# Kernel tuning notes

Measured on AMD Instinct MI355X. Metric: run time of the kernel, lower is better.

## Reference

```python
import jax, jax.numpy as jnp
import numpy as np

POOLING_COUNTS = [15, 8, 8]
N_GRID = 64


def _build_plan(pooling_counts, n):
    """Return list of (kernel_size, conv_stride, i_idx, j_idx) matching torch module order."""
    plan = []
    stride, offset = 1, 0
    for gi, c in enumerate(pooling_counts):
        for k in range(c):
            offset += stride
            i = np.arange(0, n - offset, stride)
            j = np.arange(offset, n, stride)
            ksz = 3 if (gi > 0 and k == 0) else 2
            cstride = 2 if ksz == 3 else 1
            plan.append((ksz, cstride, i, j))
        stride *= 2
    return plan


def _conv1d(x, w, b, stride):
    # x: [B, C, L], w: [O, I, K]
    y = jax.lax.conv_general_dilated(
        x, w, window_strides=(stride,), padding='VALID',
        dimension_numbers=('NCH', 'OIH', 'NCH'))
    return y + b[None, :, None]


def setup_inputs() -> dict:
    key = jax.random.key(0)
    ks = jax.random.split(key, 5)
    H = 256
    x = jax.random.normal(ks[0], (32, H, N_GRID), dtype=jnp.float32)
    w2 = jax.random.normal(ks[1], (29, H, H, 2), dtype=jnp.float32) * 0.03
    b2 = jnp.zeros((29, H), dtype=jnp.float32)
    w3 = jax.random.normal(ks[2], (2, H, H, 3), dtype=jnp.float32) * 0.03
    b3 = jnp.zeros((2, H), dtype=jnp.float32)
    vis_w = jax.random.normal(ks[3], (H, 3 * H), dtype=jnp.float32) * 0.03
    vis_b = jnp.zeros((H,), dtype=jnp.float32)
    return {"x": x, "w2": w2, "b2": b2, "w3": w3, "b3": b3,
            "vis_w": vis_w, "vis_b": vis_b}


def reference(x, w2, b2, w3, b3, vis_w, vis_b):
    plan = _build_plan(POOLING_COUNTS, N_GRID)
    B, D, n = x.shape
    diag = np.arange(n)
    src = x
    map2d = jnp.zeros((B, 3 * D, n, n), dtype=x.dtype)
    map2d = map2d.at[:, :, diag, diag].set(jnp.tile(x, (1, 3, 1)))
    cur = x
    i2 = i3 = 0
    for ksz, cstride, ii, jj in plan:
        if ksz == 2:
            w, b = w2[i2], b2[i2]; i2 += 1
        else:
            w, b = w3[i3], b3[i3]; i3 += 1
        cur = _conv1d(cur, w, b, cstride)          # [B, D, len(ii)]
        feat = jnp.concatenate([src[:, :, ii], cur, src[:, :, jj]], axis=1)
        map2d = map2d.at[:, :, ii, jj].set(feat)
    # 1x1 Conv2d(3D -> D)
    out = jnp.einsum('bcij,oc->boij', map2d, vis_w) + vis_b[None, :, None, None]
    return out
```

## Files before the change

### kernel.cpp

```cpp
#include <hip/hip_runtime.h>

#define BB 32
#define NSTEP 31
#define CROW 1040
#define CB_STRIDE 266240L
#define XB_STRIDE 16384L
#define PPART 524288L

static const int h_lens[NSTEP] = {63,62,61,60,59,58,57,56,55,54,53,52,51,50,49,
                                  24,23,22,21,20,19,18,17,
                                  8,7,6,5,4,3,2,1};
static const int h_cb[NSTEP]   = {0,63,125,186,246,305,363,420,476,531,585,638,690,741,791,
                                  840,864,887,909,930,950,969,987,
                                  1004,1012,1019,1025,1030,1034,1037,1039};

__device__ __constant__ int d_cb[NSTEP] = {0,63,125,186,246,305,363,420,476,531,585,638,690,741,791,
                                           840,864,887,909,930,950,969,987,
                                           1004,1012,1019,1025,1030,1034,1037,1039};

typedef short v8s __attribute__((ext_vector_type(8)));
typedef float v4f __attribute__((ext_vector_type(4)));

__device__ __forceinline__ unsigned short rne_bf16(float f) {
    unsigned int u = __float_as_uint(f);
    u = (u + 0x7FFFu + ((u >> 16) & 1u)) >> 16;
    return (unsigned short)u;
}

__global__ __launch_bounds__(256)
void prep(const float* __restrict__ x, const float* __restrict__ w2,
          const float* __restrict__ w3, const float* __restrict__ vw,
          unsigned short* __restrict__ xb, unsigned short* __restrict__ w2t,
          unsigned short* __restrict__ w3t, unsigned short* __restrict__ vwb)
{
    long idx = (long)blockIdx.x * 256 + threadIdx.x;
    if (idx < 524288) {
        const int ci = idx & 255, l = (idx >> 8) & 63, b = (int)(idx >> 14);
        xb[idx] = rne_bf16(x[((long)b << 14) + ((long)ci << 6) + l]);
        return;
    }
    idx -= 524288;
    if (idx < 3801088) {
        const int ci = idx & 255, k = (idx >> 8) & 1; const long row = idx >> 9;
        w2t[idx] = rne_bf16(w2[row * 512 + ci * 2 + k]);
        return;
    }
    idx -= 3801088;
    if (idx < 393216) {
        const int ci = idx & 255; const long r = idx >> 8;
        const int k = (int)(r % 3); const long row = r / 3;
        w3t[idx] = rne_bf16(w3[row * 768 + ci * 3 + k]);
        return;
    }
    idx -= 393216;
    if (idx < 196608) vwb[idx] = rne_bf16(vw[idx]);
}

template<int KC, int S, int OMODE>
__global__ __launch_bounds__(256)
void mg(const unsigned short* __restrict__ A, int arow, int acol0,
        const unsigned short* __restrict__ B, long bbstr, int brow0,
        const float* __restrict__ bias,
        void* __restrict__ OUT, int orow0)
{
    const int lane = threadIdx.x & 63;
    const int wave = threadIdx.x >> 6;
    const int nl = lane & 15, g = lane >> 4;
    const int n = blockIdx.x * 16 + nl;
    const int b = n & 31;
    const int l = n >> 5;
    const int p = blockIdx.y;

    const unsigned short* Ab = A + (size_t)(wave * 64 + nl) * arow + acol0 + p * 256 + g * 8;
    const unsigned short* Bb = B + (size_t)b * bbstr + (size_t)(brow0 + l * S) * 256 + g * 8;

    v4f acc[4] = {};
    #pragma unroll
    for (int k = 0; k < KC * 8; ++k) {
        const v8s bf = *(const v8s*)(Bb + k * 32);
        #pragma unroll
        for (int mf = 0; mf < 4; ++mf) {
            const v8s af = *(const v8s*)(Ab + (size_t)mf * 16 * arow + k * 32);
            acc[mf] = __builtin_amdgcn_mfma_f32_16x16x32_bf16(af, bf, acc[mf], 0, 0, 0);
        }
    }

    #pragma unroll
    for (int mf = 0; mf < 4; ++mf) {
        const int m0 = wave * 64 + mf * 16 + g * 4;
        if constexpr (OMODE == 0) {
            const float4 bv = *(const float4*)(bias + m0);
            ushort4 pk;
            pk.x = rne_bf16(acc[mf][0] + bv.x);
            pk.y = rne_bf16(acc[mf][1] + bv.y);
            pk.z = rne_bf16(acc[mf][2] + bv.z);
            pk.w = rne_bf16(acc[mf][3] + bv.w);
            *(ushort4*)((unsigned short*)OUT + (size_t)b * CB_STRIDE + (size_t)(orow0 + l) * 256 + m0) = pk;
        } else if constexpr (OMODE == 1) {
            *(v4f*)((float*)OUT + (size_t)b * CB_STRIDE + (size_t)l * 256 + m0) = acc[mf];
        } else {
            float* Po = (float*)OUT + (size_t)p * PPART + (size_t)b * XB_STRIDE + l;
            #pragma unroll
            for (int r = 0; r < 4; ++r) Po[(size_t)(m0 + r) * 64] = acc[mf][r];
        }
    }
}

__global__ __launch_bounds__(256)
void final_k(const float* __restrict__ P, const float* __restrict__ Qb,
             const float* __restrict__ vb, float* __restrict__ out)
{
    const int b = blockIdx.x >> 6;
    const int i = blockIdx.x & 63;
    const int t = threadIdx.x;
    const int j = t & 63;
    const int os = t >> 6;

    __shared__ int qidx[64];
    if (t < 64) {
        const int d = t - i;
        int v = -1;
        if (t == i) v = -2;
        else if (d >= 1 && d <= 15) v = d_cb[d-1] + i;
        else if (d >= 17 && d <= 31 && (d & 1) && !(i & 1)) v = d_cb[15 + ((d-17)>>1)] + (i>>1);
        else if (d >= 35 && d <= 63 && ((d-35)&3)==0 && !(i&3)) v = d_cb[23 + ((d-35)>>2)] + (i>>2);
        qidx[t] = v;
    }
    __syncthreads();
    const int q = qidx[j];

    for (int oc = 0; oc < 64; ++oc) {
        const int o = oc * 4 + os;
        const float pl = P[(size_t)(b * 256 + o) * 64 + i];
        const float pm = P[524288u + (size_t)(b * 256 + o) * 64 + i];
        const float* pr = P + 1048576u + (size_t)(b * 256 + o) * 64;
        const float vbv = vb[o];
        float v;
        if (q == -2)      v = pl + pm + pr[i] + vbv;
        else if (q >= 0)  v = pl + Qb[(size_t)b * CB_STRIDE + (size_t)q * 256 + o] + pr[j] + vbv;
        else              v = vbv;
        out[(((size_t)b * 256 + o) * 64 + i) * 64 + j] = v;
    }
}

extern "C" void kernel_launch(void* const* d_in, const int* in_sizes, int n_in,
                              void* d_out, int out_size, void* d_ws, size_t ws_size,
                              hipStream_t stream)
{
    const float* x   = (const float*)d_in[0];
    const float* w2  = (const float*)d_in[1];
    const float* b2  = (const float*)d_in[2];
    const float* w3  = (const float*)d_in[3];
    const float* b3  = (const float*)d_in[4];
    const float* vw  = (const float*)d_in[5];
    const float* vb  = (const float*)d_in[6];
    float* out = (float*)d_out;

    char* w = (char*)d_ws;
    float*          Qf  = (float*)w;                  w += (size_t)BB * CB_STRIDE * 4;
    float*          P   = (float*)w;                  w += (size_t)3 * PPART * 4;
    unsigned short* Cb  = (unsigned short*)w;         w += (size_t)BB * CB_STRIDE * 2;
    unsigned short* xb  = (unsigned short*)w;         w += (size_t)BB * XB_STRIDE * 2;
    unsigned short* w2t = (unsigned short*)w;         w += (size_t)29 * 256 * 512 * 2;
    unsigned short* w3t = (unsigned short*)w;         w += (size_t)2 * 256 * 768 * 2;
    unsigned short* vwb = (unsigned short*)w;

    prep<<<dim3(19200), 256, 0, stream>>>(x, w2, w3, vw, xb, w2t, w3t, vwb);

    mg<1,1,2><<<dim3(128, 3), 256, 0, stream>>>(vwb, 768, 0, xb, XB_STRIDE, 0, nullptr, P, 0);

    int i2 = 0, i3 = 0;
    for (int t = 0; t < NSTEP; ++t) {
        const int L = h_lens[t];
        const unsigned short* Bsrc = (t == 0) ? xb : Cb;
        const long bst  = (t == 0) ? XB_STRIDE : CB_STRIDE;
        const int brow0 = (t == 0) ? 0 : h_cb[t-1];
        if (t == 15 || t == 23) {
            mg<3,2,0><<<dim3(2*L, 1), 256, 0, stream>>>(
                w3t + (size_t)i3 * 196608, 768, 0, Bsrc, bst, brow0,
                b3 + i3 * 256, Cb, h_cb[t]);
            ++i3;
        } else {
            mg<2,1,0><<<dim3(2*L, 1), 256, 0, stream>>>(
                w2t + (size_t)i2 * 131072, 512, 0, Bsrc, bst, brow0,
                b2 + i2 * 256, Cb, h_cb[t]);
            ++i2;
        }
    }

    mg<1,1,1><<<dim3(2080, 1), 256, 0, stream>>>(vwb, 768, 256, Cb, CB_STRIDE, 0, nullptr, Qf, 0);

    final_k<<<dim3(BB * 64), 256, 0, stream>>>(P, Qf, vb, out);
}
```

Before: 625.7 us.

## Fuse the conv chain, P and Q GEMMs into one persistent per-batch kernel

Replaces the 31 per-step conv launches plus the separate P and Q GEMM launches with a single kernel: one 1024-thread block per batch element. The block keeps its activations in double-buffered, XOR-swizzled LDS and runs every conv step and its Q projection in place. This removes launch overhead and the global round trips of intermediate activations. The cost is that only 32 blocks run, which underuses the GPU's compute units and serialises the steps within each block.

```diff
diff --git a/kernel.cpp b/kernel.cpp
--- a/kernel.cpp
+++ b/kernel.cpp
@@ -4,16 +4,11 @@
 #define NSTEP 31
 #define CROW 1040
 #define CB_STRIDE 266240L
-#define XB_STRIDE 16384L
 #define PPART 524288L
 
-static const int h_lens[NSTEP] = {63,62,61,60,59,58,57,56,55,54,53,52,51,50,49,
-                                  24,23,22,21,20,19,18,17,
-                                  8,7,6,5,4,3,2,1};
-static const int h_cb[NSTEP]   = {0,63,125,186,246,305,363,420,476,531,585,638,690,741,791,
-                                  840,864,887,909,930,950,969,987,
-                                  1004,1012,1019,1025,1030,1034,1037,1039};
-
+__device__ __constant__ int d_lens[NSTEP] = {63,62,61,60,59,58,57,56,55,54,53,52,51,50,49,
+                                             24,23,22,21,20,19,18,17,
+                                             8,7,6,5,4,3,2,1};
 __device__ __constant__ int d_cb[NSTEP] = {0,63,125,186,246,305,363,420,476,531,585,638,690,741,791,
                                            840,864,887,909,930,950,969,987,
                                            1004,1012,1019,1025,1030,1034,1037,1039};
@@ -56,53 +51,155 @@
     if (idx < 196608) vwb[idx] = rne_bf16(vw[idx]);
 }
 
-template<int KC, int S, int OMODE>
-__global__ __launch_bounds__(256)
-void mg(const unsigned short* __restrict__ A, int arow, int acol0,
-        const unsigned short* __restrict__ B, long bbstr, int brow0,
-        const float* __restrict__ bias,
-        void* __restrict__ OUT, int orow0)
-{
-    const int lane = threadIdx.x & 63;
-    const int wave = threadIdx.x >> 6;
-    const int nl = lane & 15, g = lane >> 4;
-    const int n = blockIdx.x * 16 + nl;
-    const int b = n & 31;
-    const int l = n >> 5;
-    const int p = blockIdx.y;
-
-    const unsigned short* Ab = A + (size_t)(wave * 64 + nl) * arow + acol0 + p * 256 + g * 8;
-    const unsigned short* Bb = B + (size_t)b * bbstr + (size_t)(brow0 + l * S) * 256 + g * 8;
-
-    v4f acc[4] = {};
-    #pragma unroll
-    for (int k = 0; k < KC * 8; ++k) {
-        const v8s bf = *(const v8s*)(Bb + k * 32);
+
+template<int KC, int S>
+__device__ __forceinline__ void conv_step(
+    const unsigned short* __restrict__ Wt, const float* __restrict__ bias,
+    const char* __restrict__ in, char* __restrict__ out,
+    int L, int wave, int nl, int g)
+{
+    const int nt = (L + 15) >> 4;
+    v4f acc[4] = {{0,0,0,0},{0,0,0,0},{0,0,0,0},{0,0,0,0}};
+    int lv[4];
+    #pragma unroll
+    for (int j = 0; j < 4; ++j) lv[j] = min(j * 16 + nl, L - 1);
+
+    const unsigned short* Arow = Wt + (size_t)(wave * 16 + nl) * (KC * 256) + g * 8;
+    #pragma unroll
+    for (int ki = 0; ki < KC * 8; ++ki) {
+        const int kk = ki * 32;
+        const v8s af = *(const v8s*)(Arow + kk);
         #pragma unroll
-        for (int mf = 0; mf < 4; ++mf) {
-            const v8s af = *(const v8s*)(Ab + (size_t)mf * 16 * arow + k * 32);
-            acc[mf] = __builtin_amdgcn_mfma_f32_16x16x32_bf16(af, bf, acc[mf], 0, 0, 0);
-        }
-    }
-
-    #pragma unroll
-    for (int mf = 0; mf < 4; ++mf) {
-        const int m0 = wave * 64 + mf * 16 + g * 4;
-        if constexpr (OMODE == 0) {
-            const float4 bv = *(const float4*)(bias + m0);
+        for (int j = 0; j < 4; ++j) {
+            if (j < nt) {
+                const int ir = lv[j] * S + (kk >> 8);
+                const v8s bf = *(const v8s*)(in + ir * 512 +
+                                (((kk & 255) * 2 + g * 16) ^ ((ir & 7) << 4)));
+                acc[j] = __builtin_amdgcn_mfma_f32_16x16x32_bf16(af, bf, acc[j], 0, 0, 0);
+            }
+        }
+    }
+    const int m0 = wave * 16 + g * 4;
+    const float4 bv = *(const float4*)(bias + m0);
+    #pragma unroll
+    for (int j = 0; j < 4; ++j) {
+        const int l = j * 16 + nl;
+        if (j < nt && l < L) {
             ushort4 pk;
-            pk.x = rne_bf16(acc[mf][0] + bv.x);
-            pk.y = rne_bf16(acc[mf][1] + bv.y);
-            pk.z = rne_bf16(acc[mf][2] + bv.z);
-            pk.w = rne_bf16(acc[mf][3] + bv.w);
-            *(ushort4*)((unsigned short*)OUT + (size_t)b * CB_STRIDE + (size_t)(orow0 + l) * 256 + m0) = pk;
-        } else if constexpr (OMODE == 1) {
-            *(v4f*)((float*)OUT + (size_t)b * CB_STRIDE + (size_t)l * 256 + m0) = acc[mf];
+            pk.x = rne_bf16(acc[j][0] + bv.x);
+            pk.y = rne_bf16(acc[j][1] + bv.y);
+            pk.z = rne_bf16(acc[j][2] + bv.z);
+            pk.w = rne_bf16(acc[j][3] + bv.w);
+            *(ushort4*)(out + l * 512 + ((m0 * 2) ^ ((l & 7) << 4))) = pk;
+        }
+    }
+}
+
+__device__ __forceinline__ void q_step(
+    const unsigned short* __restrict__ vwb,
+    const char* __restrict__ act, float* __restrict__ Qf,
+    int b, int row0, int L, int wave, int nl, int g)
+{
+    const int nt = (L + 15) >> 4;
+    v4f acc[4] = {{0,0,0,0},{0,0,0,0},{0,0,0,0},{0,0,0,0}};
+    int lv[4];
+    #pragma unroll
+    for (int j = 0; j < 4; ++j) lv[j] = min(j * 16 + nl, L - 1);
+
+    const unsigned short* Arow = vwb + (size_t)(wave * 16 + nl) * 768 + 256 + g * 8;
+    #pragma unroll
+    for (int ki = 0; ki < 8; ++ki) {
+        const int kk = ki * 32;
+        const v8s af = *(const v8s*)(Arow + kk);
+        #pragma unroll
+        for (int j = 0; j < 4; ++j) {
+            if (j < nt) {
+                const int ir = lv[j];
+                const v8s bf = *(const v8s*)(act + ir * 512 +
+                                ((kk * 2 + g * 16) ^ ((ir & 7) << 4)));
+                acc[j] = __builtin_amdgcn_mfma_f32_16x16x32_bf16(af, bf, acc[j], 0, 0, 0);
+            }
+        }
+    }
+    const int m0 = wave * 16 + g * 4;
+    #pragma unroll
+    for (int j = 0; j < 4; ++j) {
+        const int l = j * 16 + nl;
+        if (j < nt && l < L)
+            *(v4f*)(Qf + (size_t)b * CB_STRIDE + (size_t)(row0 + l) * 256 + m0) = acc[j];
+    }
+}
+
+__global__ __launch_bounds__(1024, 4)
+void chain(const unsigned short* __restrict__ xb,
+           const unsigned short* __restrict__ w2t,
+           const unsigned short* __restrict__ w3t,
+           const unsigned short* __restrict__ vwb,
+           const float* __restrict__ b2, const float* __restrict__ b3,
+           float* __restrict__ Qf, float* __restrict__ P)
+{
+    __shared__ unsigned short lds[2][64][256];
+    const int b = blockIdx.x;
+    const int tid = threadIdx.x;
+    const int wave = tid >> 6, lane = tid & 63, nl = lane & 15, g = lane >> 4;
+
+    char* base = (char*)&lds[0][0][0];
+
+    {
+        const unsigned short* src = xb + (size_t)b * 16384;
+        #pragma unroll
+        for (int i = 0; i < 2; ++i) {
+            const int c = tid + i * 1024;
+            const int r = c >> 5, cc = c & 31;
+            const v8s v = *(const v8s*)(src + r * 256 + cc * 8);
+            *(v8s*)(base + r * 512 + ((cc * 16) ^ ((r & 7) << 4))) = v;
+        }
+    }
+    __syncthreads();
+
+    {
+        const char* in = base;
+        for (int p = 0; p < 3; ++p) {
+            v4f acc[4] = {{0,0,0,0},{0,0,0,0},{0,0,0,0},{0,0,0,0}};
+            #pragma unroll
+            for (int ki = 0; ki < 8; ++ki) {
+                const int kk = ki * 32;
+                const v8s af = *(const v8s*)(vwb + (size_t)(wave * 16 + nl) * 768 + p * 256 + kk + g * 8);
+                #pragma unroll
+                for (int j = 0; j < 4; ++j) {
+                    const int l = j * 16 + nl;
+                    const v8s bf = *(const v8s*)(in + l * 512 +
+                                    ((kk * 2 + g * 16) ^ ((l & 7) << 4)));
+                    acc[j] = __builtin_amdgcn_mfma_f32_16x16x32_bf16(af, bf, acc[j], 0, 0, 0);
+                }
+            }
+            const int m0 = wave * 16 + g * 4;
+            #pragma unroll
+            for (int j = 0; j < 4; ++j) {
+                float* po = P + (size_t)p * PPART + (size_t)b * 16384 + j * 16 + nl;
+                #pragma unroll
+                for (int r = 0; r < 4; ++r) po[(size_t)(m0 + r) * 64] = acc[j][r];
+            }
+        }
+    }
+
+    int cur = 0, i2 = 0, i3 = 0;
+    for (int t = 0; t < NSTEP; ++t) {
+        const int L = d_lens[t];
+        char* inb  = base + cur * 32768;
+        char* outb = base + (cur ^ 1) * 32768;
+        if (t == 15 || t == 23) {
+            conv_step<3, 2>(w3t + (size_t)i3 * 196608, b3 + i3 * 256,
+                            inb, outb, L, wave, nl, g);
+            ++i3;
         } else {
-            float* Po = (float*)OUT + (size_t)p * PPART + (size_t)b * XB_STRIDE + l;
-            #pragma unroll
-            for (int r = 0; r < 4; ++r) Po[(size_t)(m0 + r) * 64] = acc[mf][r];
-        }
+            conv_step<2, 1>(w2t + (size_t)i2 * 131072, b2 + i2 * 256,
+                            inb, outb, L, wave, nl, g);
+            ++i2;
+        }
+        __syncthreads();
+        q_step(vwb, outb, Qf, b, d_cb[t], L, wave, nl, g);
+        cur ^= 1;
     }
 }
 
@@ -157,38 +254,14 @@
     float* out = (float*)d_out;
 
     char* w = (char*)d_ws;
-    float*          Qf  = (float*)w;                  w += (size_t)BB * CB_STRIDE * 4;
-    float*          P   = (float*)w;                  w += (size_t)3 * PPART * 4;
-    unsigned short* Cb  = (unsigned short*)w;         w += (size_t)BB * CB_STRIDE * 2;
-    unsigned short* xb  = (unsigned short*)w;         w += (size_t)BB * XB_STRIDE * 2;
-    unsigned short* w2t = (unsigned short*)w;         w += (size_t)29 * 256 * 512 * 2;
-    unsigned short* w3t = (unsigned short*)w;         w += (size_t)2 * 256 * 768 * 2;
+    float*          Qf  = (float*)w;          w += (size_t)BB * CB_STRIDE * 4;
+    float*          P   = (float*)w;          w += (size_t)3 * PPART * 4;
+    unsigned short* xb  = (unsigned short*)w; w += (size_t)BB * 16384 * 2;
+    unsigned short* w2t = (unsigned short*)w; w += (size_t)29 * 131072 * 2;
+    unsigned short* w3t = (unsigned short*)w; w += (size_t)2 * 196608 * 2;
     unsigned short* vwb = (unsigned short*)w;
 
     prep<<<dim3(19200), 256, 0, stream>>>(x, w2, w3, vw, xb, w2t, w3t, vwb);
-
-    mg<1,1,2><<<dim3(128, 3), 256, 0, stream>>>(vwb, 768, 0, xb, XB_STRIDE, 0, nullptr, P, 0);
-
-    int i2 = 0, i3 = 0;
-    for (int t = 0; t < NSTEP; ++t) {
-        const int L = h_lens[t];
-        const unsigned short* Bsrc = (t == 0) ? xb : Cb;
-        const long bst  = (t == 0) ? XB_STRIDE : CB_STRIDE;
-        const int brow0 = (t == 0) ? 0 : h_cb[t-1];
-        if (t == 15 || t == 23) {
-            mg<3,2,0><<<dim3(2*L, 1), 256, 0, stream>>>(
-                w3t + (size_t)i3 * 196608, 768, 0, Bsrc, bst, brow0,
-                b3 + i3 * 256, Cb, h_cb[t]);
-            ++i3;
-        } else {
-            mg<2,1,0><<<dim3(2*L, 1), 256, 0, stream>>>(
-                w2t + (size_t)i2 * 131072, 512, 0, Bsrc, bst, brow0,
-                b2 + i2 * 256, Cb, h_cb[t]);
-            ++i2;
-        }
-    }
-
-    mg<1,1,1><<<dim3(2080, 1), 256, 0, stream>>>(vwb, 768, 256, Cb, CB_STRIDE, 0, nullptr, Qf, 0);
-
+    chain<<<dim3(BB), 1024, 0, stream>>>(xb, w2t, w3t, vwb, b2, b3, Qf, P);
     final_k<<<dim3(BB * 64), 256, 0, stream>>>(P, Qf, vb, out);
 }
```

Result: slower. 812.5 us (+29.9%).

## Fuse 31-step conv chain into one persistent per-batch kernel with LDS ping-pong

Applied to the files above, without the earlier changes.

Replaces the 31 separate conv launches with a single kernel that runs one 1024-thread block per batch element, keeping the activation sequence in double-buffered LDS and iterating all steps with block barriers. Each step still writes its bf16 output to global Cb for the later 1x1 projection. This removes per-step launch overhead and global round-trips for the chain input, but uses only 32 blocks on a many-CU GPU and has every block re-read all weights from global/L2.

```diff
diff --git a/kernel.cpp b/kernel.cpp
--- a/kernel.cpp
+++ b/kernel.cpp
@@ -6,14 +6,12 @@
 #define CB_STRIDE 266240L
 #define XB_STRIDE 16384L
 #define PPART 524288L
-
-static const int h_lens[NSTEP] = {63,62,61,60,59,58,57,56,55,54,53,52,51,50,49,
-                                  24,23,22,21,20,19,18,17,
-                                  8,7,6,5,4,3,2,1};
-static const int h_cb[NSTEP]   = {0,63,125,186,246,305,363,420,476,531,585,638,690,741,791,
-                                  840,864,887,909,930,950,969,987,
-                                  1004,1012,1019,1025,1030,1034,1037,1039};
-
+#define RS 528
+#define BUF (64 * RS)
+
+__device__ __constant__ int d_lens[NSTEP] = {63,62,61,60,59,58,57,56,55,54,53,52,51,50,49,
+                                             24,23,22,21,20,19,18,17,
+                                             8,7,6,5,4,3,2,1};
 __device__ __constant__ int d_cb[NSTEP] = {0,63,125,186,246,305,363,420,476,531,585,638,690,741,791,
                                            840,864,887,909,930,950,969,987,
                                            1004,1012,1019,1025,1030,1034,1037,1039};
@@ -25,6 +23,12 @@
     unsigned int u = __float_as_uint(f);
     u = (u + 0x7FFFu + ((u >> 16) & 1u)) >> 16;
     return (unsigned short)u;
+}
+
+#define MFMA16 __builtin_amdgcn_mfma_f32_16x16x32_bf16
+
+__device__ __forceinline__ void lds_barrier() {
+    asm volatile("s_waitcnt lgkmcnt(0)\n\ts_barrier" ::: "memory");
 }
 
 __global__ __launch_bounds__(256)
@@ -56,12 +60,181 @@
     if (idx < 196608) vwb[idx] = rne_bf16(vw[idx]);
 }
 
-template<int KC, int S, int OMODE>
+
+template<int KC, int S>
+__device__ __forceinline__ void conv_big(
+    const unsigned short* __restrict__ Wt, const float* __restrict__ bias,
+    const char* in, char* out, unsigned short* __restrict__ Cbp,
+    int L, int wave, int nl, int g)
+{
+    const int wm = wave >> 1;
+    const int lg2 = wave & 1;
+    const int l0 = lg2 * 32 + nl, l1 = l0 + 16;
+    const int lv0 = min(l0, L - 1), lv1 = min(l1, L - 1);
+
+    v4f a00 = {0,0,0,0}, a01 = {0,0,0,0}, a10 = {0,0,0,0}, a11 = {0,0,0,0};
+    const unsigned short* A0 = Wt + (size_t)(wm * 32 + nl) * (KC * 256) + g * 8;
+    const unsigned short* A1 = A0 + (size_t)16 * (KC * 256);
+
+    #pragma unroll
+    for (int c = 0; c < KC; ++c) {
+        v8s wf0[8], wf1[8];
+        #pragma unroll
+        for (int k = 0; k < 8; ++k) {
+            wf0[k] = *(const v8s*)(A0 + (c * 8 + k) * 32);
+            wf1[k] = *(const v8s*)(A1 + (c * 8 + k) * 32);
+        }
+        const char* rp0 = in + (lv0 * S + c) * RS + g * 16;
+        const char* rp1 = in + (lv1 * S + c) * RS + g * 16;
+        #pragma unroll
+        for (int k = 0; k < 8; ++k) {
+            const v8s b0 = *(const v8s*)(rp0 + k * 64);
+            const v8s b1 = *(const v8s*)(rp1 + k * 64);
+            a00 = MFMA16(wf0[k], b0, a00, 0, 0, 0);
+            a10 = MFMA16(wf1[k], b0, a10, 0, 0, 0);
+            a01 = MFMA16(wf0[k], b1, a01, 0, 0, 0);
+            a11 = MFMA16(wf1[k], b1, a11, 0, 0, 0);
+        }
+    }
+    const int m0 = wm * 32 + g * 4;
+    const float4 bv0 = *(const float4*)(bias + m0);
+    const float4 bv1 = *(const float4*)(bias + m0 + 16);
+    #pragma unroll
+    for (int li = 0; li < 2; ++li) {
+        const int l = li ? l1 : l0;
+        if (l < L) {
+            const v4f aa = li ? a01 : a00;
+            const v4f ab = li ? a11 : a10;
+            ushort4 p0, p1;
+            p0.x = rne_bf16(aa[0] + bv0.x); p0.y = rne_bf16(aa[1] + bv0.y);
+            p0.z = rne_bf16(aa[2] + bv0.z); p0.w = rne_bf16(aa[3] + bv0.w);
+            p1.x = rne_bf16(ab[0] + bv1.x); p1.y = rne_bf16(ab[1] + bv1.y);
+            p1.z = rne_bf16(ab[2] + bv1.z); p1.w = rne_bf16(ab[3] + bv1.w);
+            *(ushort4*)(out + l * RS + m0 * 2) = p0;
+            *(ushort4*)(out + l * RS + (m0 + 16) * 2) = p1;
+            *(ushort4*)(Cbp + (size_t)l * 256 + m0) = p0;
+            *(ushort4*)(Cbp + (size_t)l * 256 + m0 + 16) = p1;
+        }
+    }
+}
+
+template<int KC, int S, bool TWO_L>
+__device__ __forceinline__ void conv_small(
+    const unsigned short* __restrict__ Wt, const float* __restrict__ bias,
+    const char* in, char* out, unsigned short* __restrict__ Cbp,
+    int L, int wave, int nl, int g)
+{
+    const int lv0 = min(nl, L - 1);
+    const int lv1 = min(16 + nl, L - 1);
+
+    v4f a0 = {0,0,0,0}, a1 = {0,0,0,0};
+    const unsigned short* A0 = Wt + (size_t)(wave * 16 + nl) * (KC * 256) + g * 8;
+
+    #pragma unroll
+    for (int c = 0; c < KC; ++c) {
+        v8s wf[8];
+        #pragma unroll
+        for (int k = 0; k < 8; ++k)
+            wf[k] = *(const v8s*)(A0 + (c * 8 + k) * 32);
+        const char* rp0 = in + (lv0 * S + c) * RS + g * 16;
+        const char* rp1 = in + (lv1 * S + c) * RS + g * 16;
+        #pragma unroll
+        for (int k = 0; k < 8; ++k) {
+            const v8s b0 = *(const v8s*)(rp0 + k * 64);
+            a0 = MFMA16(wf[k], b0, a0, 0, 0, 0);
+            if (TWO_L) {
+                const v8s b1 = *(const v8s*)(rp1 + k * 64);
+                a1 = MFMA16(wf[k], b1, a1, 0, 0, 0);
+            }
+        }
+    }
+    const int m0 = wave * 16 + g * 4;
+    const float4 bv = *(const float4*)(bias + m0);
+    {
+        const int l = nl;
+        if (l < L) {
+            ushort4 pk;
+            pk.x = rne_bf16(a0[0] + bv.x); pk.y = rne_bf16(a0[1] + bv.y);
+            pk.z = rne_bf16(a0[2] + bv.z); pk.w = rne_bf16(a0[3] + bv.w);
+            *(ushort4*)(out + l * RS + m0 * 2) = pk;
+            *(ushort4*)(Cbp + (size_t)l * 256 + m0) = pk;
+        }
+    }
+    if (TWO_L) {
+        const int l = 16 + nl;
+        if (l < L) {
+            ushort4 pk;
+            pk.x = rne_bf16(a1[0] + bv.x); pk.y = rne_bf16(a1[1] + bv.y);
+            pk.z = rne_bf16(a1[2] + bv.z); pk.w = rne_bf16(a1[3] + bv.w);
+            *(ushort4*)(out + l * RS + m0 * 2) = pk;
+            *(ushort4*)(Cbp + (size_t)l * 256 + m0) = pk;
+        }
+    }
+}
+
+__global__ __launch_bounds__(1024, 4)
+void chain(const unsigned short* __restrict__ xb,
+           const unsigned short* __restrict__ w2t,
+           const unsigned short* __restrict__ w3t,
+           const float* __restrict__ b2, const float* __restrict__ b3,
+           unsigned short* __restrict__ Cb)
+{
+    __shared__ __align__(16) char lds[2 * BUF];
+    const int b = blockIdx.x;
+    const int tid = threadIdx.x;
+    const int wave = tid >> 6, lane = tid & 63, nl = lane & 15, g = lane >> 4;
+
+    char* base = lds;
+
+    {
+        const unsigned short* src = xb + (size_t)b * XB_STRIDE;
+        #pragma unroll
+        for (int i = 0; i < 2; ++i) {
+            const int c = tid + i * 1024;
+            const int r = c >> 5, cc = c & 31;
+            const v8s v = *(const v8s*)(src + r * 256 + cc * 8);
+            *(v8s*)(base + r * RS + cc * 16) = v;
+        }
+    }
+    lds_barrier();
+
+    unsigned short* Cbb = Cb + (size_t)b * CB_STRIDE;
+    int cur = 0, i2 = 0, i3 = 0;
+    for (int t = 0; t < NSTEP; ++t) {
+        const int L = d_lens[t];
+        char* inb  = base + cur * BUF;
+        char* outb = base + (cur ^ 1) * BUF;
+        unsigned short* Cbp = Cbb + (size_t)d_cb[t] * 256;
+        if (t < 15) {
+            conv_big<2, 1>(w2t + (size_t)i2 * 131072, b2 + i2 * 256,
+                           inb, outb, Cbp, L, wave, nl, g);
+            ++i2;
+        } else if (t == 15) {
+            conv_small<3, 2, true>(w3t, b3, inb, outb, Cbp, L, wave, nl, g);
+            ++i3;
+        } else if (t < 23) {
+            conv_small<2, 1, true>(w2t + (size_t)i2 * 131072, b2 + i2 * 256,
+                                   inb, outb, Cbp, L, wave, nl, g);
+            ++i2;
+        } else if (t == 23) {
+            conv_small<3, 2, false>(w3t + 196608, b3 + 256,
+                                    inb, outb, Cbp, L, wave, nl, g);
+            ++i3;
+        } else {
+            conv_small<2, 1, false>(w2t + (size_t)i2 * 131072, b2 + i2 * 256,
+                                    inb, outb, Cbp, L, wave, nl, g);
+            ++i2;
+        }
+        lds_barrier();
+        cur ^= 1;
+    }
+}
+
+template<int OMODE>
 __global__ __launch_bounds__(256)
 void mg(const unsigned short* __restrict__ A, int arow, int acol0,
-        const unsigned short* __restrict__ B, long bbstr, int brow0,
-        const float* __restrict__ bias,
-        void* __restrict__ OUT, int orow0)
+        const unsigned short* __restrict__ B, long bbstr,
+        void* __restrict__ OUT)
 {
     const int lane = threadIdx.x & 63;
     const int wave = threadIdx.x >> 6;
@@ -72,31 +245,22 @@
     const int p = blockIdx.y;
 
     const unsigned short* Ab = A + (size_t)(wave * 64 + nl) * arow + acol0 + p * 256 + g * 8;
-    const unsigned short* Bb = B + (size_t)b * bbstr + (size_t)(brow0 + l * S) * 256 + g * 8;
+    const unsigned short* Bb = B + (size_t)b * bbstr + (size_t)l * 256 + g * 8;
 
     v4f acc[4] = {};
     #pragma unroll
-    for (int k = 0; k < KC * 8; ++k) {
+    for (int k = 0; k < 8; ++k) {
         const v8s bf = *(const v8s*)(Bb + k * 32);
         #pragma unroll
         for (int mf = 0; mf < 4; ++mf) {
             const v8s af = *(const v8s*)(Ab + (size_t)mf * 16 * arow + k * 32);
-            acc[mf] = __builtin_amdgcn_mfma_f32_16x16x32_bf16(af, bf, acc[mf], 0, 0, 0);
-        }
-    }
-
+            acc[mf] = MFMA16(af, bf, acc[mf], 0, 0, 0);
+        }
+    }
     #pragma unroll
     for (int mf = 0; mf < 4; ++mf) {
         const int m0 = wave * 64 + mf * 16 + g * 4;
-        if constexpr (OMODE == 0) {
-            const float4 bv = *(const float4*)(bias + m0);
-            ushort4 pk;
-            pk.x = rne_bf16(acc[mf][0] + bv.x);
-            pk.y = rne_bf16(acc[mf][1] + bv.y);
-            pk.z = rne_bf16(acc[mf][2] + bv.z);
-            pk.w = rne_bf16(acc[mf][3] + bv.w);
-            *(ushort4*)((unsigned short*)OUT + (size_t)b * CB_STRIDE + (size_t)(orow0 + l) * 256 + m0) = pk;
-        } else if constexpr (OMODE == 1) {
+        if constexpr (OMODE == 1) {
             *(v4f*)((float*)OUT + (size_t)b * CB_STRIDE + (size_t)l * 256 + m0) = acc[mf];
         } else {
             float* Po = (float*)OUT + (size_t)p * PPART + (size_t)b * XB_STRIDE + l;
@@ -157,38 +321,17 @@
     float* out = (float*)d_out;
 
     char* w = (char*)d_ws;
-    float*          Qf  = (float*)w;                  w += (size_t)BB * CB_STRIDE * 4;
-    float*          P   = (float*)w;                  w += (size_t)3 * PPART * 4;
-    unsigned short* Cb  = (unsigned short*)w;         w += (size_t)BB * CB_STRIDE * 2;
-    unsigned short* xb  = (unsigned short*)w;         w += (size_t)BB * XB_STRIDE * 2;
-    unsigned short* w2t = (unsigned short*)w;         w += (size_t)29 * 256 * 512 * 2;
-    unsigned short* w3t = (unsigned short*)w;         w += (size_t)2 * 256 * 768 * 2;
+    float*          Qf  = (float*)w;          w += (size_t)BB * CB_STRIDE * 4;
+    float*          P   = (float*)w;          w += (size_t)3 * PPART * 4;
+    unsigned short* Cb  = (unsigned short*)w; w += (size_t)BB * CB_STRIDE * 2;
+    unsigned short* xb  = (unsigned short*)w; w += (size_t)BB * XB_STRIDE * 2;
+    unsigned short* w2t = (unsigned short*)w; w += (size_t)29 * 131072 * 2;
+    unsigned short* w3t = (unsigned short*)w; w += (size_t)2 * 196608 * 2;
     unsigned short* vwb = (unsigned short*)w;
 
     prep<<<dim3(19200), 256, 0, stream>>>(x, w2, w3, vw, xb, w2t, w3t, vwb);
-
-    mg<1,1,2><<<dim3(128, 3), 256, 0, stream>>>(vwb, 768, 0, xb, XB_STRIDE, 0, nullptr, P, 0);
-
-    int i2 = 0, i3 = 0;
-    for (int t = 0; t < NSTEP; ++t) {
-        const int L = h_lens[t];
-        const unsigned short* Bsrc = (t == 0) ? xb : Cb;
-        const long bst  = (t == 0) ? XB_STRIDE : CB_STRIDE;
-        const int brow0 = (t == 0) ? 0 : h_cb[t-1];
-        if (t == 15 || t == 23) {
-            mg<3,2,0><<<dim3(2*L, 1), 256, 0, stream>>>(
-                w3t + (size_t)i3 * 196608, 768, 0, Bsrc, bst, brow0,
-                b3 + i3 * 256, Cb, h_cb[t]);
-            ++i3;
-        } else {
-            mg<2,1,0><<<dim3(2*L, 1), 256, 0, stream>>>(
-                w2t + (size_t)i2 * 131072, 512, 0, Bsrc, bst, brow0,
-                b2 + i2 * 256, Cb, h_cb[t]);
-            ++i2;
-        }
-    }
-
-    mg<1,1,1><<<dim3(2080, 1), 256, 0, stream>>>(vwb, 768, 256, Cb, CB_STRIDE, 0, nullptr, Qf, 0);
-
+    mg<2><<<dim3(128, 3), 256, 0, stream>>>(vwb, 768, 0, xb, XB_STRIDE, P);
+    chain<<<dim3(BB), 1024, 0, stream>>>(xb, w2t, w3t, b2, b3, Cb);
+    mg<1><<<dim3(2080, 1), 256, 0, stream>>>(vwb, 768, 256, Cb, CB_STRIDE, Qf);
     final_k<<<dim3(BB * 64), 256, 0, stream>>>(P, Qf, vb, out);
 }
```

New measurement: 635.3 us. Within noise of the previous version (+1.5%).
